# Optimization experiments

Hardware: AMD Instinct MI355X
Metric: run time of the kernel (lower is better)

## Reference

```python
import jax, jax.numpy as jnp
from jax import lax
import numpy as np
import math

IMG_H, IMG_W = 592, 800  # stride-16 image for a 50x37 feature map


def _make_anchors(fx=50, fy=37, base=8, dsr=16):
    rows = []
    for x in range(fx):
        for y in range(fy):
            for size in [base, 2 * base, 4 * base]:
                rows.append([(x - size / 2) * dsr, (y - size / 2) * dsr,
                             (x + size / 2) * dsr, (y + size / 2) * dsr])
                s = math.sqrt(size ** 2 / 2)
                rows.append([(x - s) * dsr, (y - s / 2) * dsr, (x + s) * dsr, (y + s / 2) * dsr])
                rows.append([(x - s / 2) * dsr, (y - s) * dsr, (x + s / 2) * dsr, (y + s) * dsr])
    return np.array(rows, np.float32)


def setup_inputs() -> dict:
    key = jax.random.key(0)
    k = jax.random.split(key, 8)
    B, G, H, W = 32, 20, 50, 37
    feats = jax.random.normal(k[0], (B, 512, H, W), jnp.float32)
    a = _make_anchors()
    keep = (a[:, 0] >= 0) & (a[:, 1] >= 0) & (a[:, 2] <= IMG_W) & (a[:, 3] <= IMG_H)
    idxs_inside = jnp.asarray(np.nonzero(keep)[0].astype(np.int32))
    anchors = jnp.asarray(a[keep])
    # valid xyxy GT boxes inside the image
    x1 = jax.random.uniform(k[1], (B, G)) * (IMG_W - 160)
    y1 = jax.random.uniform(k[2], (B, G)) * (IMG_H - 160)
    w = 32.0 + jax.random.uniform(k[3], (B, G)) * 96.0
    h = 32.0 + jax.random.uniform(k[4], (B, G)) * 96.0
    gt_boxes = jnp.stack([x1, y1, x1 + w, y1 + h], -1)
    W3 = jax.random.normal(k[5], (512, 512, 3, 3), jnp.float32) * 0.02
    b3 = jnp.zeros((512,), jnp.float32)
    Wcls = jax.random.normal(k[6], (18, 512, 1, 1), jnp.float32) * 0.02
    bcls = jnp.zeros((18,), jnp.float32)
    Wloc = jax.random.normal(k[7], (36, 512, 1, 1), jnp.float32) * 0.02
    bloc = jnp.zeros((36,), jnp.float32)
    return {"feats": feats, "gt_boxes": gt_boxes, "anchors": anchors,
            "W3": W3, "b3": b3, "Wcls": Wcls, "bcls": bcls,
            "Wloc": Wloc, "bloc": bloc, "idxs_inside": idxs_inside}


def _conv(x, w, b, pad):
    y = lax.conv_general_dilated(x, w, (1, 1), pad,
                                 dimension_numbers=("NCHW", "OIHW", "NCHW"))
    return y + b[None, :, None, None]


def reference(feats, gt_boxes, anchors, W3, b3, Wcls, bcls, Wloc, bloc, idxs_inside):
    B = feats.shape[0]
    rpn_conv1 = jax.nn.relu(_conv(feats, W3, b3, "SAME"))
    cls_score = _conv(rpn_conv1, Wcls, bcls, "VALID")          # [B,18,H,W]
    _, C, H, Wd = cls_score.shape
    logits = cls_score.reshape(B, 2, (C * H) // 2, Wd)          # reshape(x, 2)
    prob = jax.nn.softmax(logits, axis=1)
    prob_back = prob.reshape(B, C, H, Wd)                       # reshape back to 18
    loc_pred = _conv(rpn_conv1, Wloc, bloc, "VALID")            # [B,36,H,W]

    # select inside-image anchors
    logits_sel = logits.transpose(0, 2, 3, 1).reshape(B, -1, 2)[:, idxs_inside, :]
    loc_sel = loc_pred.transpose(0, 2, 3, 1).reshape(B, -1, 4)[:, idxs_inside, :]

    # vectorized anchors x gt IoU (replaces the triple python loop)
    ix1 = jnp.maximum(anchors[None, :, None, 0], gt_boxes[:, None, :, 0])
    iy1 = jnp.maximum(anchors[None, :, None, 1], gt_boxes[:, None, :, 1])
    ix2 = jnp.minimum(anchors[None, :, None, 2], gt_boxes[:, None, :, 2])
    iy2 = jnp.minimum(anchors[None, :, None, 3], gt_boxes[:, None, :, 3])
    inter = jnp.clip(ix2 - ix1, 0) * jnp.clip(iy2 - iy1, 0)     # [B,A,G]
    area_a = (anchors[:, 2] - anchors[:, 0]) * (anchors[:, 3] - anchors[:, 1])
    area_g = (gt_boxes[..., 2] - gt_boxes[..., 0]) * (gt_boxes[..., 3] - gt_boxes[..., 1])
    iou = inter / jnp.maximum(area_a[None, :, None] + area_g[:, None, :] - inter, 1e-8)

    max_iou = iou.max(-1)                                       # [B,A]
    matched = iou.argmax(-1)                                    # [B,A] gt index per anchor
    gt_best = iou.argmax(1)                                     # [B,G] best anchor per gt
    A = anchors.shape[0]
    is_best = jnp.zeros((B, A), bool).at[jnp.arange(B)[:, None], gt_best].set(True)
    labels = (is_best | (max_iou > 0.7)).astype(jnp.int32)      # positives=1, rest 0

    logsm = jax.nn.log_softmax(logits_sel, -1)
    loss_cls = -jnp.take_along_axis(logsm, labels[..., None], -1).mean()

    tgt = jnp.take_along_axis(gt_boxes, matched[:, :, None], axis=1)  # [B,A,4]
    d = loc_sel - tgt
    sl1 = jnp.where(jnp.abs(d) < 1.0, 0.5 * d * d, jnp.abs(d) - 0.5)
    loss_loc = (sl1 * labels[..., None].astype(sl1.dtype)).sum() / 256.0

    return prob_back, loc_pred, loss_cls, loss_loc
```

## Files before the change

kernel.cpp:

```cpp
#include <hip/hip_runtime.h>
#include <stdint.h>

typedef unsigned short u16;
typedef unsigned int   u32;
typedef unsigned long long u64;

typedef __bf16 v8bf __attribute__((ext_vector_type(8)));
typedef float  v4f  __attribute__((ext_vector_type(4)));

#define NBATCH 32
#define NCH    512
#define FH     50
#define FW     37
#define PIX    1850
#define MTOT   59200
#define KTOT   4608
#define HP     52
#define WP     39
#define NG     20
#define W3N    (NCH*KTOT)

#define PROB_N 1065600
#define LOC_N  2131200
#define LC_IDX 3196800
#define LL_IDX 3196801

__device__ __forceinline__ u16 f2bf(float f) {
    u32 u = __float_as_uint(f);
    u += 0x7fffu + ((u >> 16) & 1u);
    return (u16)(u >> 16);
}
__device__ __forceinline__ float bf_lo(u32 u){ return __uint_as_float(u << 16); }
__device__ __forceinline__ float bf_hi(u32 u){ return __uint_as_float(u & 0xffff0000u); }

__device__ __forceinline__ void gl_lds16(const u16* g, u16* l) {
    __builtin_amdgcn_global_load_lds((const __attribute__((address_space(1))) u32*)g,
                                     (__attribute__((address_space(3))) u32*)l,
                                     16, 0, 0);
}

__global__ __launch_bounds__(256) void pad_kernel(const float* __restrict__ feats,
                                                  u16* __restrict__ fpad) {
    __shared__ float t[64][65];
    const int b  = blockIdx.z;
    const int c0 = blockIdx.y * 64;
    const int p0 = blockIdx.x * 64;
    const int tid = threadIdx.x;
    {
        const int cl = tid >> 2, seg = tid & 3;
        const float* src = feats + ((size_t)b * NCH + c0 + cl) * PIX;
        const int pbase = p0 + seg * 16;
        #pragma unroll
        for (int i = 0; i < 16; i++) {
            int p = pbase + i;
            t[cl][seg * 16 + i] = (p < PIX) ? src[p] : 0.f;
        }
    }
    __syncthreads();
    {
        const int pl = tid >> 2, cs = tid & 3;
        const int p = p0 + pl;
        if (p < PIX) {
            const int h = p / FW, w = p % FW;
            size_t dst = (((size_t)b * HP + h + 1) * WP + (w + 1)) * NCH + c0 + cs * 16;
            u32 pk[8];
            #pragma unroll
            for (int i = 0; i < 8; i++) {
                u32 lo = f2bf(t[cs * 16 + 2 * i][pl]);
                u32 hi = f2bf(t[cs * 16 + 2 * i + 1][pl]);
                pk[i] = lo | (hi << 16);
            }
            *(uint4*)&fpad[dst]     = make_uint4(pk[0], pk[1], pk[2], pk[3]);
            *(uint4*)&fpad[dst + 8] = make_uint4(pk[4], pk[5], pk[6], pk[7]);
        }
    }
}

__global__ __launch_bounds__(256) void border_kernel(u16* __restrict__ fpad) {
    int t = blockIdx.x * 256 + threadIdx.x;
    int c8 = t & 63;
    int pi = (t >> 6) % 178;
    int b  = (t >> 6) / 178;
    int h, w;
    if (pi < 39)       { h = 0;        w = pi; }
    else if (pi < 78)  { h = 51;       w = pi - 39; }
    else if (pi < 128) { h = pi - 77;  w = 0; }
    else               { h = pi - 127; w = 38; }
    size_t dst = (((size_t)b * HP + h) * WP + w) * NCH + c8 * 8;
    *(uint4*)&fpad[dst] = make_uint4(0, 0, 0, 0);
}

__global__ void wprep(const float* __restrict__ w3, const float* __restrict__ wcls,
                      const float* __restrict__ wloc,
                      u16* __restrict__ wbt, u16* __restrict__ wcb) {
    int t = blockIdx.x * 256 + threadIdx.x;
    if (t < W3N) {
        int co = t / KTOT, k = t % KTOT;
        int dydx = k >> 9, ci = k & 511;
        wbt[t] = f2bf(w3[((size_t)co * NCH + ci) * 9 + dydx]);
    } else {
        int t2 = t - W3N;
        if (t2 < 54 * 512) {
            int c = t2 >> 9, ci = t2 & 511;
            float v = (c < 18) ? wcls[c * 512 + ci] : wloc[(c - 18) * 512 + ci];
            wcb[t2] = f2bf(v);
        }
    }
}

__global__ __launch_bounds__(256) void conv3x3_mfma(const u16* __restrict__ fpad,
                                                    const u16* __restrict__ wbt,
                                                    const float* __restrict__ b3,
                                                    u16* __restrict__ conv1) {
    __shared__ __align__(16) u16 As[128][64];
    __shared__ __align__(16) u16 Bs[128][64];

    const int lid = blockIdx.x;
    const int xcd = lid & 7;
    const int n_idx = (lid >> 3) & 3;
    const int m_idx = xcd * 58 + (lid >> 5);
    if (m_idx >= 463) return;
    const int m_base = m_idx * 128;
    const int n_base = n_idx * 128;

    const int tid = threadIdx.x;
    const int wave = tid >> 6;
    const int lane = tid & 63;

    const int srow  = tid >> 3;
    const int seg_g = (tid & 7) ^ (srow & 7);

    int rbA[4];
    #pragma unroll
    for (int r = 0; r < 4; r++) {
        int m = m_base + r * 32 + srow;
        int mm = (m < MTOT) ? m : 0;
        int b = mm / PIX, p = mm % PIX;
        int y = p / FW, x = p % FW;
        rbA[r] = ((b * HP + y) * WP + x) * NCH + seg_g * 8;
    }
    int rbB[4];
    #pragma unroll
    for (int r = 0; r < 4; r++) {
        int n = n_base + r * 32 + srow;
        rbB[r] = n * KTOT + seg_g * 8;
    }

    u16* const asb = &As[0][0] + wave * 512;
    u16* const bsb = &Bs[0][0] + wave * 512;

    const int wm = (wave >> 1) * 64;
    const int wn = (wave & 1) * 64;
    const int lm = lane & 15;
    const int quad = lane >> 4;
    const int x7 = lm & 7;

    v4f acc[4][4];
    #pragma unroll
    for (int i = 0; i < 4; i++)
        #pragma unroll
        for (int j = 0; j < 4; j++)
            #pragma unroll
            for (int r = 0; r < 4; r++) acc[i][j][r] = 0.f;

    for (int k0 = 0; k0 < KTOT; k0 += 64) {
        const int dydx = k0 >> 9;
        const int ci0  = k0 & 511;
        const int offA = ((dydx / 3) * WP + (dydx % 3)) * NCH + ci0;
        #pragma unroll
        for (int r = 0; r < 4; r++)
            gl_lds16(fpad + rbA[r] + offA, asb + r * 2048);
        #pragma unroll
        for (int r = 0; r < 4; r++)
            gl_lds16(wbt + rbB[r] + k0, bsb + r * 2048);
        __syncthreads();

        #pragma unroll
        for (int kh = 0; kh < 2; kh++) {
            const int ps = (((kh << 2) | quad) ^ x7) * 8;
            v8bf af[4], bfv[4];
            #pragma unroll
            for (int i = 0; i < 4; i++)
                af[i]  = *(const v8bf*)(&As[0][0] + (wm + i * 16 + lm) * 64 + ps);
            #pragma unroll
            for (int i = 0; i < 4; i++)
                bfv[i] = *(const v8bf*)(&Bs[0][0] + (wn + i * 16 + lm) * 64 + ps);
            #pragma unroll
            for (int i = 0; i < 4; i++)
                #pragma unroll
                for (int j = 0; j < 4; j++)
                    acc[i][j] = __builtin_amdgcn_mfma_f32_16x16x32_bf16(af[i], bfv[j], acc[i][j], 0, 0, 0);
        }
        __syncthreads();
    }

    #pragma unroll
    for (int j = 0; j < 4; j++) {
        const int n = n_base + wn + j * 16 + lm;
        const float bias = b3[n];
        #pragma unroll
        for (int i = 0; i < 4; i++) {
            #pragma unroll
            for (int r = 0; r < 4; r++) {
                int m = m_base + wm + i * 16 + quad * 4 + r;
                if (m < MTOT) {
                    float v = acc[i][j][r] + bias;
                    v = v > 0.f ? v : 0.f;
                    conv1[(size_t)m * NCH + n] = f2bf(v);
                }
            }
        }
    }
}

__global__ __launch_bounds__(256) void head_kernel(const u16* __restrict__ conv1,
                                                   const u16* __restrict__ wcb,
                                                   const float* __restrict__ bcls,
                                                   const float* __restrict__ bloc,
                                                   float* __restrict__ out) {
    __shared__ __align__(16) u16 xl[4][520];
    __shared__ float cls_l[4][18];
    const int tid = threadIdx.x;
    const int m0 = blockIdx.x * 4;
    {
        const int r = tid & 3;
        const int kk = (tid >> 2) * 8;
        *(uint4*)&xl[r][kk] = *(const uint4*)&conv1[(size_t)(m0 + r) * NCH + kk];
    }
    __syncthreads();
    const int c = tid >> 2;
    const int pix = tid & 3;
    float a0 = 0.f, a1 = 0.f, a2 = 0.f, a3 = 0.f;
    if (c < 54) {
        const uint4* wp = (const uint4*)(wcb + c * 512);
        #pragma unroll 8
        for (int it = 0; it < 64; it++) {
            uint4 xv = *(const uint4*)&xl[pix][it * 8];
            uint4 wv = wp[it];
            a0 = fmaf(bf_lo(xv.x), bf_lo(wv.x), a0);
            a1 = fmaf(bf_hi(xv.x), bf_hi(wv.x), a1);
            a2 = fmaf(bf_lo(xv.y), bf_lo(wv.y), a2);
            a3 = fmaf(bf_hi(xv.y), bf_hi(wv.y), a3);
            a0 = fmaf(bf_lo(xv.z), bf_lo(wv.z), a0);
            a1 = fmaf(bf_hi(xv.z), bf_hi(wv.z), a1);
            a2 = fmaf(bf_lo(xv.w), bf_lo(wv.w), a2);
            a3 = fmaf(bf_hi(xv.w), bf_hi(wv.w), a3);
        }
    }
    float acc = (a0 + a1) + (a2 + a3);
    const int m = m0 + pix;
    const int b = m / PIX;
    const int p = m % PIX;
    if (c >= 18 && c < 54) {
        out[(size_t)PROB_N + ((size_t)b * 36 + (c - 18)) * PIX + p] = acc + bloc[c - 18];
    }
    if (c < 18) cls_l[pix][c] = acc + bcls[c];
    __syncthreads();
    if (c < 9) {
        float s0 = cls_l[pix][c], s1 = cls_l[pix][c + 9];
        float mx = fmaxf(s0, s1);
        float e0 = expf(s0 - mx), e1 = expf(s1 - mx);
        float inv = 1.f / (e0 + e1);
        out[((size_t)b * 18 + c) * PIX + p]     = e0 * inv;
        out[((size_t)b * 18 + c + 9) * PIX + p] = e1 * inv;
    }
}

__global__ __launch_bounds__(256) void iou_kernel(const float* __restrict__ anchors,
                                                  const float* __restrict__ gtb,
                                                  int A,
                                                  float* __restrict__ max_iou,
                                                  int* __restrict__ matched,
                                                  u64* __restrict__ gtkey) {
    __shared__ float g[NG * 4];
    __shared__ u64 wk[4][NG];
    const int b = blockIdx.y;
    const int tid = threadIdx.x;
    if (tid < NG * 4) g[tid] = gtb[b * NG * 4 + tid];
    __syncthreads();
    const int a = blockIdx.x * 256 + tid;
    const bool act = a < A;
    const int aa = act ? a : 0;
    const float ax1 = anchors[aa * 4 + 0], ay1 = anchors[aa * 4 + 1];
    const float ax2 = anchors[aa * 4 + 2], ay2 = anchors[aa * 4 + 3];
    const float areaA = (ax2 - ax1) * (ay2 - ay1);
    float best = -1.f;
    int bg = 0;
    const int lane = tid & 63, wave = tid >> 6;
    for (int gi = 0; gi < NG; gi++) {
        float gx1 = g[gi * 4], gy1 = g[gi * 4 + 1], gx2 = g[gi * 4 + 2], gy2 = g[gi * 4 + 3];
        float iw = fmaxf(fminf(ax2, gx2) - fmaxf(ax1, gx1), 0.f);
        float ih = fmaxf(fminf(ay2, gy2) - fmaxf(ay1, gy1), 0.f);
        float inter = iw * ih;
        float areaG = (gx2 - gx1) * (gy2 - gy1);
        float iou = inter / fmaxf(areaA + areaG - inter, 1e-8f);
        if (act && iou > best) { best = iou; bg = gi; }
        u64 key = act ? (((u64)__float_as_uint(iou) << 32) | (u64)(0xFFFFFFFFu - (u32)a)) : 0ull;
        #pragma unroll
        for (int off = 32; off; off >>= 1) {
            u64 o = __shfl_xor(key, off);
            key = (o > key) ? o : key;
        }
        if (lane == 0) wk[wave][gi] = key;
    }
    if (act) {
        max_iou[(size_t)b * A + a] = best;
        matched[(size_t)b * A + a] = bg;
    }
    __syncthreads();
    if (tid < NG) {
        u64 k = wk[0][tid];
        k = (wk[1][tid] > k) ? wk[1][tid] : k;
        k = (wk[2][tid] > k) ? wk[2][tid] : k;
        k = (wk[3][tid] > k) ? wk[3][tid] : k;
        atomicMax(&gtkey[b * NG + tid], k);
    }
}

__global__ __launch_bounds__(256) void loss_kernel(const float* __restrict__ gtb,
                                                   const int* __restrict__ idxs,
                                                   const float* __restrict__ max_iou,
                                                   const int* __restrict__ matched,
                                                   const u64* __restrict__ gtkey,
                                                   int A,
                                                   float* out) {
    __shared__ float g[NG * 4];
    __shared__ int gbest[NG];
    __shared__ float red[8];
    const int b = blockIdx.y;
    const int tid = threadIdx.x;
    if (tid < NG * 4) g[tid] = gtb[b * NG * 4 + tid];
    if (tid < NG) {
        u64 k = gtkey[b * NG + tid];
        gbest[tid] = (int)(0xFFFFFFFFu - (u32)(k & 0xFFFFFFFFull));
    }
    __syncthreads();
    const int a = blockIdx.x * 256 + tid;
    float lc = 0.f, ll = 0.f;
    if (a < A) {
        float mi = max_iou[(size_t)b * A + a];
        int lbl = (mi > 0.7f) ? 1 : 0;
        if (!lbl) {
            #pragma unroll
            for (int gi = 0; gi < NG; gi++) lbl |= (gbest[gi] == a);
        }
        const int idx = idxs[a];
        const int cpr = idx / PIX;
        const int rem = idx % PIX;
        float p0 = out[((size_t)b * 18 + cpr) * PIX + rem];
        float p1 = out[((size_t)b * 18 + cpr + 9) * PIX + rem];
        float pl = lbl ? p1 : p0;
        lc = -logf(pl);
        if (lbl) {
            const int mg = matched[(size_t)b * A + a];
            const int hh = idx / 333;
            const int r2 = idx % 333;
            const int ww = r2 / 9;
            const int c4 = r2 % 9;
            const int pp = hh * FW + ww;
            #pragma unroll
            for (int t = 0; t < 4; t++) {
                float lv = out[(size_t)PROB_N + ((size_t)b * 36 + c4 * 4 + t) * PIX + pp];
                float d = lv - g[mg * 4 + t];
                float ad = fabsf(d);
                ll += (ad < 1.f) ? 0.5f * d * d : ad - 0.5f;
            }
        }
    }
    #pragma unroll
    for (int off = 32; off; off >>= 1) {
        lc += __shfl_xor(lc, off);
        ll += __shfl_xor(ll, off);
    }
    const int lane = tid & 63, wave = tid >> 6;
    if (lane == 0) { red[wave] = lc; red[4 + wave] = ll; }
    __syncthreads();
    if (tid == 0) {
        float slc = red[0] + red[1] + red[2] + red[3];
        float sll = red[4] + red[5] + red[6] + red[7];
        atomicAdd(&out[LC_IDX], slc * (1.f / (32.f * (float)A)));
        atomicAdd(&out[LL_IDX], sll * (1.f / 256.f));
    }
}

extern "C" void kernel_launch(void* const* d_in, const int* in_sizes, int n_in,
                              void* d_out, int out_size, void* d_ws, size_t ws_size,
                              hipStream_t stream) {
    const float* feats   = (const float*)d_in[0];
    const float* gtb     = (const float*)d_in[1];
    const float* anchors = (const float*)d_in[2];
    const float* W3      = (const float*)d_in[3];
    const float* b3      = (const float*)d_in[4];
    const float* Wcls    = (const float*)d_in[5];
    const float* bcls    = (const float*)d_in[6];
    const float* Wloc    = (const float*)d_in[7];
    const float* bloc    = (const float*)d_in[8];
    const int*   idxs    = (const int*)d_in[9];
    const int A = in_sizes[9];
    float* out = (float*)d_out;

    char* ws = (char*)d_ws;
    size_t off = 0;
    auto alloc = [&](size_t bytes) -> void* {
        void* p = ws + off;
        off = (off + bytes + 255) & ~(size_t)255;
        return p;
    };
    const size_t fpad_n = (size_t)NBATCH * HP * WP * NCH;
    u16* fpad   = (u16*)alloc(fpad_n * 2);
    u16* wbt    = (u16*)alloc((size_t)NCH * KTOT * 2);
    u16* wcb    = (u16*)alloc((size_t)54 * 512 * 2);
    u16* conv1  = (u16*)alloc((size_t)MTOT * NCH * 2);
    u64* gtkey  = (u64*)alloc((size_t)NBATCH * NG * 8);
    float* max_iou = (float*)alloc((size_t)NBATCH * A * 4);
    int*   matched = (int*)alloc((size_t)NBATCH * A * 4);

    hipMemsetAsync(gtkey, 0, (size_t)NBATCH * NG * 8, stream);
    hipMemsetAsync(out + LC_IDX, 0, 8, stream);

    border_kernel<<<1424, 256, 0, stream>>>(fpad);
    pad_kernel<<<dim3(29, 8, NBATCH), 256, 0, stream>>>(feats, fpad);
    wprep<<<(W3N + 54 * 512 + 255) / 256, 256, 0, stream>>>(W3, Wcls, Wloc, wbt, wcb);
    conv3x3_mfma<<<1856, 256, 0, stream>>>(fpad, wbt, b3, conv1);
    head_kernel<<<MTOT / 4, 256, 0, stream>>>(conv1, wcb, bcls, bloc, out);
    const int ablk = (A + 255) / 256;
    iou_kernel<<<dim3(ablk, NBATCH), 256, 0, stream>>>(anchors, gtb, A, max_iou, matched, gtkey);
    loss_kernel<<<dim3(ablk, NBATCH), 256, 0, stream>>>(gtb, idxs, max_iou, matched, gtkey, A, out);
}
```

Baseline: 846.3 us.

## Use MFMA for the 1x1 head, merge prep kernels, fuse IoU and loss

The scalar-FMA head kernel, which handled 4 pixels per block, is replaced by an MFMA GEMM over 128-pixel tiles with a 64-column zero-padded weight matrix. Results are staged in LDS before the softmax and location writes. Weight prep, border zeroing and loss-accumulator clearing are merged into one launch, which removes the memsets. IoU matching and loss move into a single kernel with one block per batch that recomputes IoU twice instead of using global scratch and atomics. That block-per-batch kernel has little parallelism (32 blocks) and may become a serial tail.

```diff
diff --git a/kernel.cpp b/kernel.cpp
--- a/kernel.cpp
+++ b/kernel.cpp
@@ -19,9 +19,10 @@
 #define WP     39
 #define NG     20
 #define W3N    (NCH*KTOT)
+#define WCBN   (64*512)
+#define BORDN  364544
 
 #define PROB_N 1065600
-#define LOC_N  2131200
 #define LC_IDX 3196800
 #define LL_IDX 3196801
 
@@ -30,8 +31,6 @@
     u += 0x7fffu + ((u >> 16) & 1u);
     return (u16)(u >> 16);
 }
-__device__ __forceinline__ float bf_lo(u32 u){ return __uint_as_float(u << 16); }
-__device__ __forceinline__ float bf_hi(u32 u){ return __uint_as_float(u & 0xffff0000u); }
 
 __device__ __forceinline__ void gl_lds16(const u16* g, u16* l) {
     __builtin_amdgcn_global_load_lds((const __attribute__((address_space(1))) u32*)g,
@@ -76,35 +75,34 @@
     }
 }
 
-__global__ __launch_bounds__(256) void border_kernel(u16* __restrict__ fpad) {
+__global__ void prep_kernel(const float* __restrict__ w3, const float* __restrict__ wcls,
+                            const float* __restrict__ wloc,
+                            u16* __restrict__ wbt, u16* __restrict__ wcb,
+                            u16* __restrict__ fpad, float* __restrict__ out) {
     int t = blockIdx.x * 256 + threadIdx.x;
-    int c8 = t & 63;
-    int pi = (t >> 6) % 178;
-    int b  = (t >> 6) / 178;
-    int h, w;
-    if (pi < 39)       { h = 0;        w = pi; }
-    else if (pi < 78)  { h = 51;       w = pi - 39; }
-    else if (pi < 128) { h = pi - 77;  w = 0; }
-    else               { h = pi - 127; w = 38; }
-    size_t dst = (((size_t)b * HP + h) * WP + w) * NCH + c8 * 8;
-    *(uint4*)&fpad[dst] = make_uint4(0, 0, 0, 0);
-}
-
-__global__ void wprep(const float* __restrict__ w3, const float* __restrict__ wcls,
-                      const float* __restrict__ wloc,
-                      u16* __restrict__ wbt, u16* __restrict__ wcb) {
-    int t = blockIdx.x * 256 + threadIdx.x;
+    if (t < 2) out[LC_IDX + t] = 0.f;
     if (t < W3N) {
         int co = t / KTOT, k = t % KTOT;
         int dydx = k >> 9, ci = k & 511;
         wbt[t] = f2bf(w3[((size_t)co * NCH + ci) * 9 + dydx]);
-    } else {
+    } else if (t < W3N + WCBN) {
         int t2 = t - W3N;
-        if (t2 < 54 * 512) {
-            int c = t2 >> 9, ci = t2 & 511;
-            float v = (c < 18) ? wcls[c * 512 + ci] : wloc[(c - 18) * 512 + ci];
-            wcb[t2] = f2bf(v);
-        }
+        int c = t2 >> 9, ci = t2 & 511;
+        float v = (c < 18) ? wcls[c * 512 + ci]
+                : (c < 54) ? wloc[(c - 18) * 512 + ci] : 0.f;
+        wcb[t2] = f2bf(v);
+    } else if (t < W3N + WCBN + BORDN) {
+        int t3 = t - (W3N + WCBN);
+        int c8 = t3 & 63;
+        int pi = (t3 >> 6) % 178;
+        int b  = (t3 >> 6) / 178;
+        int h, w;
+        if (pi < 39)       { h = 0;        w = pi; }
+        else if (pi < 78)  { h = 51;       w = pi - 39; }
+        else if (pi < 128) { h = pi - 77;  w = 0; }
+        else               { h = pi - 127; w = 38; }
+        size_t dst = (((size_t)b * HP + h) * WP + w) * NCH + c8 * 8;
+        *(uint4*)&fpad[dst] = make_uint4(0, 0, 0, 0);
     }
 }
 
@@ -213,133 +211,167 @@
     }
 }
 
-__global__ __launch_bounds__(256) void head_kernel(const u16* __restrict__ conv1,
-                                                   const u16* __restrict__ wcb,
-                                                   const float* __restrict__ bcls,
-                                                   const float* __restrict__ bloc,
-                                                   float* __restrict__ out) {
-    __shared__ __align__(16) u16 xl[4][520];
-    __shared__ float cls_l[4][18];
+__global__ __launch_bounds__(256) void head_mfma(const u16* __restrict__ conv1,
+                                                 const u16* __restrict__ wcb,
+                                                 const float* __restrict__ bcls,
+                                                 const float* __restrict__ bloc,
+                                                 float* __restrict__ out) {
+    __shared__ __align__(16) u16 As[128][64];
+    __shared__ __align__(16) u16 Bs[64][64];
+    __shared__ float ct[128][66];
+
     const int tid = threadIdx.x;
-    const int m0 = blockIdx.x * 4;
-    {
-        const int r = tid & 3;
-        const int kk = (tid >> 2) * 8;
-        *(uint4*)&xl[r][kk] = *(const uint4*)&conv1[(size_t)(m0 + r) * NCH + kk];
-    }
-    __syncthreads();
+    const int m_base = blockIdx.x * 128;
+    const int wave = tid >> 6;
+    const int lane = tid & 63;
+    const int srow  = tid >> 3;
+    const int seg_g = (tid & 7) ^ (srow & 7);
+
+    int rbA[4];
+    #pragma unroll
+    for (int r = 0; r < 4; r++) {
+        int m = m_base + r * 32 + srow;
+        int mm = (m < MTOT) ? m : 0;
+        rbA[r] = mm * NCH + seg_g * 8;
+    }
+    int rbB[2];
+    #pragma unroll
+    for (int r = 0; r < 2; r++)
+        rbB[r] = (r * 32 + srow) * NCH + seg_g * 8;
+
+    u16* const asb = &As[0][0] + wave * 512;
+    u16* const bsb = &Bs[0][0] + wave * 512;
+
+    const int wn = wave * 16;
+    const int lm = lane & 15;
+    const int quad = lane >> 4;
+    const int x7 = lm & 7;
+
+    v4f acc[8];
+    #pragma unroll
+    for (int i = 0; i < 8; i++)
+        #pragma unroll
+        for (int r = 0; r < 4; r++) acc[i][r] = 0.f;
+
+    for (int k0 = 0; k0 < NCH; k0 += 64) {
+        #pragma unroll
+        for (int r = 0; r < 4; r++)
+            gl_lds16(conv1 + rbA[r] + k0, asb + r * 2048);
+        #pragma unroll
+        for (int r = 0; r < 2; r++)
+            gl_lds16(wcb + rbB[r] + k0, bsb + r * 2048);
+        __syncthreads();
+
+        #pragma unroll
+        for (int kh = 0; kh < 2; kh++) {
+            const int ps = (((kh << 2) | quad) ^ x7) * 8;
+            v8bf bf = *(const v8bf*)(&Bs[0][0] + (wn + lm) * 64 + ps);
+            #pragma unroll
+            for (int i = 0; i < 8; i++) {
+                v8bf af = *(const v8bf*)(&As[0][0] + (i * 16 + lm) * 64 + ps);
+                acc[i] = __builtin_amdgcn_mfma_f32_16x16x32_bf16(af, bf, acc[i], 0, 0, 0);
+            }
+        }
+        __syncthreads();
+    }
+
+    const int col = wn + lm;
+    const float bias = (col < 18) ? bcls[col] : (col < 54) ? bloc[col - 18] : 0.f;
+    #pragma unroll
+    for (int i = 0; i < 8; i++)
+        #pragma unroll
+        for (int r = 0; r < 4; r++)
+            ct[i * 16 + quad * 4 + r][col] = acc[i][r] + bias;
+    __syncthreads();
+
     const int c = tid >> 2;
-    const int pix = tid & 3;
-    float a0 = 0.f, a1 = 0.f, a2 = 0.f, a3 = 0.f;
-    if (c < 54) {
-        const uint4* wp = (const uint4*)(wcb + c * 512);
-        #pragma unroll 8
-        for (int it = 0; it < 64; it++) {
-            uint4 xv = *(const uint4*)&xl[pix][it * 8];
-            uint4 wv = wp[it];
-            a0 = fmaf(bf_lo(xv.x), bf_lo(wv.x), a0);
-            a1 = fmaf(bf_hi(xv.x), bf_hi(wv.x), a1);
-            a2 = fmaf(bf_lo(xv.y), bf_lo(wv.y), a2);
-            a3 = fmaf(bf_hi(xv.y), bf_hi(wv.y), a3);
-            a0 = fmaf(bf_lo(xv.z), bf_lo(wv.z), a0);
-            a1 = fmaf(bf_hi(xv.z), bf_hi(wv.z), a1);
-            a2 = fmaf(bf_lo(xv.w), bf_lo(wv.w), a2);
-            a3 = fmaf(bf_hi(xv.w), bf_hi(wv.w), a3);
-        }
-    }
-    float acc = (a0 + a1) + (a2 + a3);
-    const int m = m0 + pix;
-    const int b = m / PIX;
-    const int p = m % PIX;
-    if (c >= 18 && c < 54) {
-        out[(size_t)PROB_N + ((size_t)b * 36 + (c - 18)) * PIX + p] = acc + bloc[c - 18];
-    }
-    if (c < 18) cls_l[pix][c] = acc + bcls[c];
-    __syncthreads();
-    if (c < 9) {
-        float s0 = cls_l[pix][c], s1 = cls_l[pix][c + 9];
-        float mx = fmaxf(s0, s1);
-        float e0 = expf(s0 - mx), e1 = expf(s1 - mx);
-        float inv = 1.f / (e0 + e1);
-        out[((size_t)b * 18 + c) * PIX + p]     = e0 * inv;
-        out[((size_t)b * 18 + c + 9) * PIX + p] = e1 * inv;
-    }
-}
-
-__global__ __launch_bounds__(256) void iou_kernel(const float* __restrict__ anchors,
-                                                  const float* __restrict__ gtb,
-                                                  int A,
-                                                  float* __restrict__ max_iou,
-                                                  int* __restrict__ matched,
-                                                  u64* __restrict__ gtkey) {
+    const int pix4 = tid & 3;
+    for (int px = pix4; px < 128; px += 4) {
+        const int m = m_base + px;
+        if (m >= MTOT) break;
+        const int b = m / PIX;
+        const int p = m - b * PIX;
+        if (c < 9) {
+            float s0 = ct[px][c], s1 = ct[px][c + 9];
+            float mx = fmaxf(s0, s1);
+            float e0 = __expf(s0 - mx), e1 = __expf(s1 - mx);
+            float inv = 1.f / (e0 + e1);
+            out[((size_t)b * 18 + c) * PIX + p]     = e0 * inv;
+            out[((size_t)b * 18 + c + 9) * PIX + p] = e1 * inv;
+        } else if (c >= 18 && c < 54) {
+            out[(size_t)PROB_N + ((size_t)b * 36 + (c - 18)) * PIX + p] = ct[px][c];
+        }
+    }
+}
+
+__global__ __launch_bounds__(256) void iouloss_kernel(const float* __restrict__ anchors,
+                                                      const float* __restrict__ gtb,
+                                                      const int* __restrict__ idxs,
+                                                      int A,
+                                                      const float* __restrict__ outr,
+                                                      float* __restrict__ out) {
     __shared__ float g[NG * 4];
-    __shared__ u64 wk[4][NG];
-    const int b = blockIdx.y;
-    const int tid = threadIdx.x;
-    if (tid < NG * 4) g[tid] = gtb[b * NG * 4 + tid];
-    __syncthreads();
-    const int a = blockIdx.x * 256 + tid;
-    const bool act = a < A;
-    const int aa = act ? a : 0;
-    const float ax1 = anchors[aa * 4 + 0], ay1 = anchors[aa * 4 + 1];
-    const float ax2 = anchors[aa * 4 + 2], ay2 = anchors[aa * 4 + 3];
-    const float areaA = (ax2 - ax1) * (ay2 - ay1);
-    float best = -1.f;
-    int bg = 0;
-    const int lane = tid & 63, wave = tid >> 6;
-    for (int gi = 0; gi < NG; gi++) {
-        float gx1 = g[gi * 4], gy1 = g[gi * 4 + 1], gx2 = g[gi * 4 + 2], gy2 = g[gi * 4 + 3];
-        float iw = fmaxf(fminf(ax2, gx2) - fmaxf(ax1, gx1), 0.f);
-        float ih = fmaxf(fminf(ay2, gy2) - fmaxf(ay1, gy1), 0.f);
-        float inter = iw * ih;
-        float areaG = (gx2 - gx1) * (gy2 - gy1);
-        float iou = inter / fmaxf(areaA + areaG - inter, 1e-8f);
-        if (act && iou > best) { best = iou; bg = gi; }
-        u64 key = act ? (((u64)__float_as_uint(iou) << 32) | (u64)(0xFFFFFFFFu - (u32)a)) : 0ull;
-        #pragma unroll
-        for (int off = 32; off; off >>= 1) {
-            u64 o = __shfl_xor(key, off);
-            key = (o > key) ? o : key;
-        }
-        if (lane == 0) wk[wave][gi] = key;
-    }
-    if (act) {
-        max_iou[(size_t)b * A + a] = best;
-        matched[(size_t)b * A + a] = bg;
-    }
-    __syncthreads();
-    if (tid < NG) {
-        u64 k = wk[0][tid];
-        k = (wk[1][tid] > k) ? wk[1][tid] : k;
-        k = (wk[2][tid] > k) ? wk[2][tid] : k;
-        k = (wk[3][tid] > k) ? wk[3][tid] : k;
-        atomicMax(&gtkey[b * NG + tid], k);
-    }
-}
-
-__global__ __launch_bounds__(256) void loss_kernel(const float* __restrict__ gtb,
-                                                   const int* __restrict__ idxs,
-                                                   const float* __restrict__ max_iou,
-                                                   const int* __restrict__ matched,
-                                                   const u64* __restrict__ gtkey,
-                                                   int A,
-                                                   float* out) {
-    __shared__ float g[NG * 4];
+    __shared__ u64 keys[NG];
     __shared__ int gbest[NG];
     __shared__ float red[8];
     const int b = blockIdx.y;
     const int tid = threadIdx.x;
     if (tid < NG * 4) g[tid] = gtb[b * NG * 4 + tid];
-    if (tid < NG) {
-        u64 k = gtkey[b * NG + tid];
-        gbest[tid] = (int)(0xFFFFFFFFu - (u32)(k & 0xFFFFFFFFull));
-    }
-    __syncthreads();
-    const int a = blockIdx.x * 256 + tid;
+    if (tid < NG) keys[tid] = 0ull;
+    __syncthreads();
+
+    u64 lk[NG];
+    #pragma unroll
+    for (int gi = 0; gi < NG; gi++) lk[gi] = 0ull;
+    for (int a = tid; a < A; a += 256) {
+        const float ax1 = anchors[a * 4 + 0], ay1 = anchors[a * 4 + 1];
+        const float ax2 = anchors[a * 4 + 2], ay2 = anchors[a * 4 + 3];
+        const float areaA = (ax2 - ax1) * (ay2 - ay1);
+        const u64 atag = (u64)(0xFFFFFFFFu - (u32)a);
+        #pragma unroll
+        for (int gi = 0; gi < NG; gi++) {
+            float gx1 = g[gi*4], gy1 = g[gi*4+1], gx2 = g[gi*4+2], gy2 = g[gi*4+3];
+            float iw = fmaxf(fminf(ax2, gx2) - fmaxf(ax1, gx1), 0.f);
+            float ih = fmaxf(fminf(ay2, gy2) - fmaxf(ay1, gy1), 0.f);
+            float inter = iw * ih;
+            float areaG = (gx2 - gx1) * (gy2 - gy1);
+            float iou = inter / fmaxf(areaA + areaG - inter, 1e-8f);
+            u64 key = (((u64)__float_as_uint(iou)) << 32) | atag;
+            if (key > lk[gi]) lk[gi] = key;
+        }
+    }
+    #pragma unroll
+    for (int gi = 0; gi < NG; gi++) {
+        u64 k = lk[gi];
+        #pragma unroll
+        for (int off = 32; off; off >>= 1) {
+            u64 o = __shfl_xor(k, off);
+            k = (o > k) ? o : k;
+        }
+        if ((tid & 63) == 0) atomicMax(&keys[gi], k);
+    }
+    __syncthreads();
+    if (tid < NG) gbest[tid] = (int)(0xFFFFFFFFu - (u32)(keys[tid] & 0xFFFFFFFFull));
+    __syncthreads();
+
     float lc = 0.f, ll = 0.f;
-    if (a < A) {
-        float mi = max_iou[(size_t)b * A + a];
-        int lbl = (mi > 0.7f) ? 1 : 0;
+    for (int a = tid; a < A; a += 256) {
+        const float ax1 = anchors[a * 4 + 0], ay1 = anchors[a * 4 + 1];
+        const float ax2 = anchors[a * 4 + 2], ay2 = anchors[a * 4 + 3];
+        const float areaA = (ax2 - ax1) * (ay2 - ay1);
+        float best = -1.f;
+        int bg = 0;
+        #pragma unroll
+        for (int gi = 0; gi < NG; gi++) {
+            float gx1 = g[gi*4], gy1 = g[gi*4+1], gx2 = g[gi*4+2], gy2 = g[gi*4+3];
+            float iw = fmaxf(fminf(ax2, gx2) - fmaxf(ax1, gx1), 0.f);
+            float ih = fmaxf(fminf(ay2, gy2) - fmaxf(ay1, gy1), 0.f);
+            float inter = iw * ih;
+            float areaG = (gx2 - gx1) * (gy2 - gy1);
+            float iou = inter / fmaxf(areaA + areaG - inter, 1e-8f);
+            if (iou > best) { best = iou; bg = gi; }
+        }
+        int lbl = (best > 0.7f) ? 1 : 0;
         if (!lbl) {
             #pragma unroll
             for (int gi = 0; gi < NG; gi++) lbl |= (gbest[gi] == a);
@@ -347,12 +379,10 @@
         const int idx = idxs[a];
         const int cpr = idx / PIX;
         const int rem = idx % PIX;
-        float p0 = out[((size_t)b * 18 + cpr) * PIX + rem];
-        float p1 = out[((size_t)b * 18 + cpr + 9) * PIX + rem];
-        float pl = lbl ? p1 : p0;
-        lc = -logf(pl);
+        float p0 = outr[((size_t)b * 18 + cpr) * PIX + rem];
+        float p1 = outr[((size_t)b * 18 + cpr + 9) * PIX + rem];
+        lc += -logf(lbl ? p1 : p0);
         if (lbl) {
-            const int mg = matched[(size_t)b * A + a];
             const int hh = idx / 333;
             const int r2 = idx % 333;
             const int ww = r2 / 9;
@@ -360,8 +390,8 @@
             const int pp = hh * FW + ww;
             #pragma unroll
             for (int t = 0; t < 4; t++) {
-                float lv = out[(size_t)PROB_N + ((size_t)b * 36 + c4 * 4 + t) * PIX + pp];
-                float d = lv - g[mg * 4 + t];
+                float lv = outr[(size_t)PROB_N + ((size_t)b * 36 + c4 * 4 + t) * PIX + pp];
+                float d = lv - g[bg * 4 + t];
                 float ad = fabsf(d);
                 ll += (ad < 1.f) ? 0.5f * d * d : ad - 0.5f;
             }
@@ -408,22 +438,14 @@
     };
     const size_t fpad_n = (size_t)NBATCH * HP * WP * NCH;
     u16* fpad   = (u16*)alloc(fpad_n * 2);
-    u16* wbt    = (u16*)alloc((size_t)NCH * KTOT * 2);
-    u16* wcb    = (u16*)alloc((size_t)54 * 512 * 2);
+    u16* wbt    = (u16*)alloc((size_t)W3N * 2);
+    u16* wcb    = (u16*)alloc((size_t)WCBN * 2);
     u16* conv1  = (u16*)alloc((size_t)MTOT * NCH * 2);
-    u64* gtkey  = (u64*)alloc((size_t)NBATCH * NG * 8);
-    float* max_iou = (float*)alloc((size_t)NBATCH * A * 4);
-    int*   matched = (int*)alloc((size_t)NBATCH * A * 4);
-
-    hipMemsetAsync(gtkey, 0, (size_t)NBATCH * NG * 8, stream);
-    hipMemsetAsync(out + LC_IDX, 0, 8, stream);
-
-    border_kernel<<<1424, 256, 0, stream>>>(fpad);
+
+    const int prep_tot = W3N + WCBN + BORDN;
+    prep_kernel<<<(prep_tot + 255) / 256, 256, 0, stream>>>(W3, Wcls, Wloc, wbt, wcb, fpad, out);
     pad_kernel<<<dim3(29, 8, NBATCH), 256, 0, stream>>>(feats, fpad);
-    wprep<<<(W3N + 54 * 512 + 255) / 256, 256, 0, stream>>>(W3, Wcls, Wloc, wbt, wcb);
     conv3x3_mfma<<<1856, 256, 0, stream>>>(fpad, wbt, b3, conv1);
-    head_kernel<<<MTOT / 4, 256, 0, stream>>>(conv1, wcb, bcls, bloc, out);
-    const int ablk = (A + 255) / 256;
-    iou_kernel<<<dim3(ablk, NBATCH), 256, 0, stream>>>(anchors, gtb, A, max_iou, matched, gtkey);
-    loss_kernel<<<dim3(ablk, NBATCH), 256, 0, stream>>>(gtb, idxs, max_iou, matched, gtkey, A, out);
-}
+    head_mfma<<<463, 256, 0, stream>>>(conv1, wcb, bcls, bloc, out);
+    iouloss_kernel<<<dim3(1, NBATCH), 256, 0, stream>>>(anchors, gtb, idxs, A, out, out);
+}
```

After: 789.1 us. 1.07x faster.
